# Kernel tuning notes

Measured on AMD Instinct MI355X. Metric: run time of the kernel, lower is better.

## Reference

```python
import jax, jax.numpy as jnp
import numpy as np

D_MODEL = 1024
HEAD = 16
EPS = 1e-6


def _norm(x, alpha, beta):
    # Faithful to NormalizeLayer: torch.std is unbiased (ddof=1); scalar alpha/bias.
    mean = jnp.mean(x, axis=-1, keepdims=True)
    std = jnp.std(x, axis=-1, ddof=1, keepdims=True)
    return alpha * ((x - mean) / (std + EPS)) + beta


def setup_inputs() -> dict:
    key = jax.random.key(0)
    ks = jax.random.split(key, 16)
    B, S, D = 4, 1024, D_MODEL
    s = 1.0 / np.sqrt(D)
    inp = {
        'x': jax.random.normal(ks[0], (B, S, D), dtype=jnp.float32),
        'mask': jnp.ones((B, 1, 1, S), dtype=jnp.int32),
        'Wq_w': jax.random.normal(ks[1], (D, D), dtype=jnp.float32) * s,
        'Wq_b': jnp.zeros((D,), dtype=jnp.float32),
        'Wk_w': jax.random.normal(ks[2], (D, D), dtype=jnp.float32) * s,
        'Wk_b': jnp.zeros((D,), dtype=jnp.float32),
        'Wv_w': jax.random.normal(ks[3], (D, D), dtype=jnp.float32) * s,
        'Wv_b': jnp.zeros((D,), dtype=jnp.float32),
        'Wo_w': jax.random.normal(ks[4], (D, D), dtype=jnp.float32) * s,
        'Wo_b': jnp.zeros((D,), dtype=jnp.float32),
        'ff1_w': jax.random.normal(ks[5], (D, D), dtype=jnp.float32) * s,
        'ff1_b': jnp.zeros((D,), dtype=jnp.float32),
        'ff2_w': jax.random.normal(ks[6], (D, D), dtype=jnp.float32) * s,
        'ff2_b': jnp.zeros((D,), dtype=jnp.float32),
        'alpha1': jnp.ones((1,), dtype=jnp.float32),
        'beta1': jnp.zeros((1,), dtype=jnp.float32),
        'alpha2': jnp.ones((1,), dtype=jnp.float32),
        'beta2': jnp.zeros((1,), dtype=jnp.float32),
    }
    return inp


def reference(x, mask, Wq_w, Wq_b, Wk_w, Wk_b, Wv_w, Wv_b, Wo_w, Wo_b,
              ff1_w, ff1_b, ff2_w, ff2_b, alpha1, beta1, alpha2, beta2):
    B, S, D = x.shape
    H = HEAD
    kd = D // H
    # QKV projections (torch Linear: y = x @ W.T + b)
    Q = (x @ Wq_w.T + Wq_b).reshape(B, S, H, kd).transpose(0, 2, 1, 3)
    K = (x @ Wk_w.T + Wk_b).reshape(B, S, H, kd).transpose(0, 2, 1, 3)
    V = (x @ Wv_w.T + Wv_b).reshape(B, S, H, kd).transpose(0, 2, 1, 3)
    score = jnp.einsum('bhqd,bhkd->bhqk', Q, K) / jnp.sqrt(jnp.float32(kd))
    score = jnp.where(mask == 0, -jnp.inf, score)
    attn = jax.nn.softmax(score, axis=-1)
    o = jnp.einsum('bhqk,bhkd->bhqd', attn, V)
    o = o.transpose(0, 2, 1, 3).reshape(B, S, D)
    attn_out = o @ Wo_w.T + Wo_b
    # residual 1 + custom norm (dropout is identity in eval / drop=0)
    x1 = _norm(x + attn_out, alpha1, beta1)
    # feed-forward: Linear -> ReLU -> Linear (both d_model x d_model)
    ff = jax.nn.relu(x1 @ ff1_w.T + ff1_b) @ ff2_w.T + ff2_b
    # residual 2 + custom norm
    return _norm(x1 + ff, alpha2, beta2)
```

## Files before the change

kernel.cpp:

```cpp
#include <hip/hip_runtime.h>


typedef __bf16 bf16x8 __attribute__((ext_vector_type(8)));
typedef float f32x4 __attribute__((ext_vector_type(4)));
typedef unsigned short ushort4v __attribute__((ext_vector_type(4)));

static __device__ __forceinline__ unsigned short f2bf(float f) {
  return __builtin_bit_cast(unsigned short, (__bf16)f);
}
static __device__ __forceinline__ float bf2f(unsigned short u) {
  return __builtin_bit_cast(float, (unsigned int)u << 16);
}

static __device__ __forceinline__ void gload_lds16(const void* g, void* l) {
  __builtin_amdgcn_global_load_lds(
      (const __attribute__((address_space(1))) unsigned int*)g,
      (__attribute__((address_space(3))) unsigned int*)l, 16, 0, 0);
}

__global__ __launch_bounds__(256)
void cvt_all(const float* __restrict__ x, const float* __restrict__ wq,
             const float* __restrict__ wk, const float* __restrict__ wv,
             const float* __restrict__ wo, const float* __restrict__ w1,
             const float* __restrict__ w2,
             unsigned short* __restrict__ x_bf, unsigned short* __restrict__ wqkv_bf,
             unsigned short* __restrict__ wo_bf, unsigned short* __restrict__ w1_bf,
             unsigned short* __restrict__ w2_bf) {
  const int y = blockIdx.y;
  const size_t MEL = 1u << 20;
  const float* src;
  unsigned short* dst;
  switch (y) {
    case 0: case 1: case 2: case 3: src = x + y * MEL; dst = x_bf + y * MEL; break;
    case 4: src = wq; dst = wqkv_bf; break;
    case 5: src = wk; dst = wqkv_bf + MEL; break;
    case 6: src = wv; dst = wqkv_bf + 2 * MEL; break;
    case 7: src = wo; dst = wo_bf; break;
    case 8: src = w1; dst = w1_bf; break;
    default: src = w2; dst = w2_bf; break;
  }
  const int i = blockIdx.x * 256 + threadIdx.x;
  const float4 v = reinterpret_cast<const float4*>(src)[i];
  ushort4v o;
  o[0] = f2bf(v.x); o[1] = f2bf(v.y); o[2] = f2bf(v.z); o[3] = f2bf(v.w);
  reinterpret_cast<ushort4v*>(dst)[i] = o;
}

template<bool RELU, int OUT_MODE>
__global__ __launch_bounds__(256, 2)
void gemm_bt(const unsigned short* __restrict__ A,
             const unsigned short* __restrict__ W,
             const float* __restrict__ bias0, const float* __restrict__ bias1,
             const float* __restrict__ bias2,
             void* __restrict__ out0, unsigned short* __restrict__ outK,
             unsigned short* __restrict__ outVt, int M, int N, int K) {
  __shared__ __align__(16) unsigned short Al[2][64][64];
  __shared__ __align__(16) unsigned short Bl[2][128][64];
  const int tid = threadIdx.x;
  const int lane = tid & 63;
  const int w = tid >> 6;
  const int wr = w >> 1, wc = w & 1;
  const int grp = lane >> 4, l15 = lane & 15;
  const long bRow = (long)blockIdx.x * 64;
  const long bCol = (long)blockIdx.y * 128;

  f32x4 acc[2][4];
#pragma unroll
  for (int m = 0; m < 2; m++)
#pragma unroll
    for (int n = 0; n < 4; n++) { f32x4 z = {0.f,0.f,0.f,0.f}; acc[m][n] = z; }

  const int srow = tid >> 3;
  const int xc = (((tid & 7) ^ (srow & 7)) << 3);
  const unsigned short* Ag0 = A + (bRow + srow) * (long)K + xc;
  const unsigned short* Ag1 = Ag0 + 32L * K;
  const unsigned short* Wg0 = W + (bCol + srow) * (long)K + xc;
  const unsigned short* Wg1 = Wg0 + 32L * K;
  const unsigned short* Wg2 = Wg0 + 64L * K;
  const unsigned short* Wg3 = Wg0 + 96L * K;

  auto stage = [&](int k0, int buf) {
    unsigned short* ldsA = &Al[buf][0][0] + w * 512;
    unsigned short* ldsB = &Bl[buf][0][0] + w * 512;
    gload_lds16(Ag0 + k0, ldsA);
    gload_lds16(Ag1 + k0, ldsA + 2048);
    gload_lds16(Wg0 + k0, ldsB);
    gload_lds16(Wg1 + k0, ldsB + 2048);
    gload_lds16(Wg2 + k0, ldsB + 4096);
    gload_lds16(Wg3 + k0, ldsB + 6144);
  };

  const int NT = K >> 6;
  stage(0, 0);
  for (int t = 0; t < NT; ++t) {
    const int cur = t & 1;
    __syncthreads();
    if (t + 1 < NT) stage((t + 1) << 6, cur ^ 1);
#pragma unroll
    for (int kk = 0; kk < 2; kk++) {
      bf16x8 af[2], bfr[4];
#pragma unroll
      for (int m = 0; m < 2; m++) {
        const int R = wr * 32 + m * 16 + l15;
        const int pos = (kk * 4 + grp) ^ (R & 7);
        af[m] = *(const bf16x8*)&Al[cur][R][pos << 3];
      }
#pragma unroll
      for (int n = 0; n < 4; n++) {
        const int R = wc * 64 + n * 16 + l15;
        const int pos = (kk * 4 + grp) ^ (R & 7);
        bfr[n] = *(const bf16x8*)&Bl[cur][R][pos << 3];
      }
#pragma unroll
      for (int m = 0; m < 2; m++)
#pragma unroll
        for (int n = 0; n < 4; n++)
          acc[m][n] = __builtin_amdgcn_mfma_f32_16x16x32_bf16(af[m], bfr[n], acc[m][n], 0, 0, 0);
    }
  }

  const float QSCL = 0.125f * 1.44269504088896340736f;
  const int seg = (OUT_MODE == 2) ? (int)(bCol >> 10) : 0;
  const float* bp = (OUT_MODE == 2) ? (seg == 0 ? bias0 : seg == 1 ? bias1 : bias2) : bias0;
#pragma unroll
  for (int n = 0; n < 4; n++) {
    const long col = bCol + wc * 64 + n * 16 + l15;
    const float bv = bp[OUT_MODE == 2 ? (col & 1023) : col];
#pragma unroll
    for (int m = 0; m < 2; m++) {
      const long row0 = bRow + wr * 32 + m * 16 + grp * 4;
#pragma unroll
      for (int r = 0; r < 4; r++) {
        float v = acc[m][n][r] + bv;
        if (RELU) v = fmaxf(v, 0.f);
        const long row = row0 + r;
        if (OUT_MODE == 1) {
          ((unsigned short*)out0)[row * (long)N + col] = f2bf(v);
        } else {
          if (seg == 0) {
            ((unsigned short*)out0)[row * 1024 + col] = f2bf(v * QSCL);
          } else if (seg == 1) {
            outK[row * 1024 + (col & 1023)] = f2bf(v);
          } else {
            const long vc = col & 1023;
            const long idx = (((row >> 10) * 16 + (vc >> 6)) << 16) + ((vc & 63) << 10) + (row & 1023);
            outVt[idx] = f2bf(v);
          }
        }
      }
    }
  }
}

__global__ __launch_bounds__(256, 2)
void attn_kernel(const unsigned short* __restrict__ Qb,
                 const unsigned short* __restrict__ Kb,
                 const unsigned short* __restrict__ Vt_g,
                 const int* __restrict__ maskp,
                 unsigned short* __restrict__ Ob) {
  const int S = 1024, D = 1024;
  __shared__ __align__(16) unsigned short Kl[2][64][64];
  __shared__ __align__(16) unsigned short Vl[2][64][64];
  __shared__ __align__(16) unsigned short Pl[128][64];
  const int tid = threadIdx.x;
  const int lane = tid & 63;
  const int w = tid >> 6;
  const int grp = lane >> 4, l15 = lane & 15;
  const int bh = blockIdx.x;
  const int qt = blockIdx.y;
  const int b = bh >> 4, h = bh & 15;
  const float NEG = -__builtin_inff();

  const int4 mv = *(const int4*)(maskp + b * S + tid * 4);
  const int allLive = __syncthreads_and(mv.x && mv.y && mv.z && mv.w);

  bf16x8 aq[2][2];
#pragma unroll
  for (int m = 0; m < 2; m++) {
    const unsigned short* Qp =
        Qb + ((size_t)(b * S + qt * 128 + w * 32 + m * 16 + l15)) * D + h * 64;
    aq[m][0] = *(const bf16x8*)(Qp + grp * 8);
    aq[m][1] = *(const bf16x8*)(Qp + 32 + grp * 8);
  }

  bf16x8 onesb;
#pragma unroll
  for (int j = 0; j < 8; j++) onesb[j] = (__bf16)1.0f;

  f32x4 acc_o[2][4];
#pragma unroll
  for (int m = 0; m < 2; m++)
#pragma unroll
    for (int f = 0; f < 4; f++) { f32x4 z = {0.f,0.f,0.f,0.f}; acc_o[m][f] = z; }
  f32x4 acc_l[2] = {{0.f,0.f,0.f,0.f}, {0.f,0.f,0.f,0.f}};
  float M = NEG;

  const int srow = tid >> 3;
  const int xc = (((tid & 7) ^ (srow & 7)) << 3);
  const unsigned short* Kg0 = Kb + ((size_t)(b * S + srow)) * D + h * 64 + xc;
  const unsigned short* Kg1 = Kg0 + 32 * (size_t)D;
  const unsigned short* Vgb = Vt_g + (((size_t)bh) << 16);
  const unsigned short* Vg0 = Vgb + (size_t)srow * S + xc;
  const unsigned short* Vg1 = Vg0 + 32 * (size_t)S;

  auto stage = [&](int kt2, int buf) {
    const size_t kb = (size_t)kt2 * 64;
    gload_lds16(Kg0 + kb * D, &Kl[buf][0][0] + w * 512);
    gload_lds16(Kg1 + kb * D, &Kl[buf][0][0] + w * 512 + 2048);
    gload_lds16(Vg0 + kb,     &Vl[buf][0][0] + w * 512);
    gload_lds16(Vg1 + kb,     &Vl[buf][0][0] + w * 512 + 2048);
  };
  stage(0, 0);

  for (int kt = 0; kt < 16; ++kt) {
    const int cur = kt & 1;
    const int kbase = kt * 64;
    __syncthreads();
    if (kt < 15) stage(kt + 1, cur ^ 1);

    f32x4 sfr[2][4];
    __builtin_amdgcn_s_setprio(1);
#pragma unroll
    for (int f = 0; f < 4; f++) {
      const int R = f * 16 + l15;
      const int p0 = (grp ^ (R & 7)) << 3;
      const int p1 = ((4 + grp) ^ (R & 7)) << 3;
      bf16x8 bk0 = *(const bf16x8*)&Kl[cur][R][p0];
      bf16x8 bk1 = *(const bf16x8*)&Kl[cur][R][p1];
#pragma unroll
      for (int m = 0; m < 2; m++) {
        f32x4 z = {0.f,0.f,0.f,0.f};
        z = __builtin_amdgcn_mfma_f32_16x16x32_bf16(aq[m][0], bk0, z, 0, 0, 0);
        z = __builtin_amdgcn_mfma_f32_16x16x32_bf16(aq[m][1], bk1, z, 0, 0, 0);
        sfr[m][f] = z;
      }
    }
    __builtin_amdgcn_s_setprio(0);

    if (!allLive) {
#pragma unroll
      for (int f = 0; f < 4; f++) {
        const float biasf = maskp[b * S + kbase + f * 16 + l15] ? 0.f : NEG;
#pragma unroll
        for (int m = 0; m < 2; m++)
#pragma unroll
          for (int r = 0; r < 4; r++) sfr[m][f][r] += biasf;
      }
    }

    float rm = sfr[0][0][0];
#pragma unroll
    for (int m = 0; m < 2; m++)
#pragma unroll
      for (int f = 0; f < 4; f++)
#pragma unroll
        for (int r = 0; r < 4; r++) rm = fmaxf(rm, sfr[m][f][r]);
    rm = fmaxf(rm, __shfl_xor(rm, 1));
    rm = fmaxf(rm, __shfl_xor(rm, 2));
    rm = fmaxf(rm, __shfl_xor(rm, 4));
    rm = fmaxf(rm, __shfl_xor(rm, 8));
    rm = fmaxf(rm, __shfl_xor(rm, 16));
    rm = fmaxf(rm, __shfl_xor(rm, 32));
    if (rm > M + 8.f) {
      const float sc = exp2f(M - rm);
      M = rm;
#pragma unroll
      for (int m = 0; m < 2; m++) {
#pragma unroll
        for (int f = 0; f < 4; f++) acc_o[m][f] *= sc;
        acc_l[m] *= sc;
      }
    }

#pragma unroll
    for (int m = 0; m < 2; m++)
#pragma unroll
      for (int f = 0; f < 4; f++)
#pragma unroll
        for (int r = 0; r < 4; r++) {
          const float p = exp2f(sfr[m][f][r] - M);
          const int q = w * 32 + m * 16 + grp * 4 + r;
          const int cchunk = (f * 2 + (l15 >> 3)) ^ (q & 7);
          ((unsigned short*)Pl)[q * 64 + (cchunk << 3) + (l15 & 7)] = f2bf(p);
        }

    bf16x8 bv0[4], bv1[4];
#pragma unroll
    for (int f = 0; f < 4; f++) {
      const int Rv = f * 16 + l15;
      bv0[f] = *(const bf16x8*)&Vl[cur][Rv][((grp ^ (Rv & 7)) << 3)];
      bv1[f] = *(const bf16x8*)&Vl[cur][Rv][(((4 + grp) ^ (Rv & 7)) << 3)];
    }

    __builtin_amdgcn_s_setprio(1);
#pragma unroll
    for (int m = 0; m < 2; m++) {
      const int Rp = w * 32 + m * 16 + l15;
      const bf16x8 ap0 = *(const bf16x8*)&Pl[Rp][((grp ^ (Rp & 7)) << 3)];
      const bf16x8 ap1 = *(const bf16x8*)&Pl[Rp][(((4 + grp) ^ (Rp & 7)) << 3)];
#pragma unroll
      for (int f = 0; f < 4; f++) {
        acc_o[m][f] = __builtin_amdgcn_mfma_f32_16x16x32_bf16(ap0, bv0[f], acc_o[m][f], 0, 0, 0);
        acc_o[m][f] = __builtin_amdgcn_mfma_f32_16x16x32_bf16(ap1, bv1[f], acc_o[m][f], 0, 0, 0);
      }
      acc_l[m] = __builtin_amdgcn_mfma_f32_16x16x32_bf16(ap0, onesb, acc_l[m], 0, 0, 0);
      acc_l[m] = __builtin_amdgcn_mfma_f32_16x16x32_bf16(ap1, onesb, acc_l[m], 0, 0, 0);
    }
    __builtin_amdgcn_s_setprio(0);
  }

#pragma unroll
  for (int m = 0; m < 2; m++)
#pragma unroll
    for (int r = 0; r < 4; r++) {
      const float inv = 1.f / acc_l[m][r];
      const int row = qt * 128 + w * 32 + m * 16 + grp * 4 + r;
#pragma unroll
      for (int f = 0; f < 4; f++) {
        const float v = acc_o[m][f][r] * inv;
        Ob[((size_t)(b * S + row)) * D + h * 64 + f * 16 + l15] = f2bf(v);
      }
    }
}

template<int AMODE, int BMODE, bool F32OUT, bool BF16OUT>
__global__ __launch_bounds__(256)
void norm_residual(const void* __restrict__ a, const void* __restrict__ bsrc,
                   const float* __restrict__ alpha, const float* __restrict__ beta,
                   float* __restrict__ out, unsigned short* __restrict__ out_bf) {
  const int D = 1024;
  const size_t base = (size_t)blockIdx.x * D + threadIdx.x * 4;
  float a0, a1, a2, a3, b0v, b1v, b2v, b3v;
  if (AMODE == 0) {
    const float4 va = *(const float4*)((const float*)a + base);
    a0 = va.x; a1 = va.y; a2 = va.z; a3 = va.w;
  } else {
    const ushort4v va = *(const ushort4v*)((const unsigned short*)a + base);
    a0 = bf2f(va[0]); a1 = bf2f(va[1]); a2 = bf2f(va[2]); a3 = bf2f(va[3]);
  }
  if (BMODE == 0) {
    const float4 vb = *(const float4*)((const float*)bsrc + base);
    b0v = vb.x; b1v = vb.y; b2v = vb.z; b3v = vb.w;
  } else {
    const ushort4v vb = *(const ushort4v*)((const unsigned short*)bsrc + base);
    b0v = bf2f(vb[0]); b1v = bf2f(vb[1]); b2v = bf2f(vb[2]); b3v = bf2f(vb[3]);
  }
  const float x0 = a0 + b0v, x1 = a1 + b1v, x2 = a2 + b2v, x3 = a3 + b3v;
  float s1 = x0 + x1 + x2 + x3;
  float s2 = x0 * x0 + x1 * x1 + x2 * x2 + x3 * x3;
#pragma unroll
  for (int m = 1; m < 64; m <<= 1) {
    s1 += __shfl_xor(s1, m);
    s2 += __shfl_xor(s2, m);
  }
  __shared__ float red[8];
  const int w = threadIdx.x >> 6, lane = threadIdx.x & 63;
  if (lane == 0) { red[w] = s1; red[4 + w] = s2; }
  __syncthreads();
  s1 = red[0] + red[1] + red[2] + red[3];
  s2 = red[4] + red[5] + red[6] + red[7];
  const float mean = s1 * (1.f / 1024.f);
  const float var = fmaxf((s2 - 1024.f * mean * mean) * (1.f / 1023.f), 0.f);
  const float k = alpha[0] / (sqrtf(var) + 1e-6f);
  const float b0 = beta[0];
  const float y0 = (x0 - mean) * k + b0;
  const float y1 = (x1 - mean) * k + b0;
  const float y2 = (x2 - mean) * k + b0;
  const float y3 = (x3 - mean) * k + b0;
  if (F32OUT) {
    float4 o = {y0, y1, y2, y3};
    *(float4*)(out + base) = o;
  }
  if (BF16OUT) {
    ushort4v ob;
    ob[0] = f2bf(y0); ob[1] = f2bf(y1); ob[2] = f2bf(y2); ob[3] = f2bf(y3);
    *(ushort4v*)(out_bf + base) = ob;
  }
}

extern "C" void kernel_launch(void* const* d_in, const int* in_sizes, int n_in,
                              void* d_out, int out_size, void* d_ws, size_t ws_size,
                              hipStream_t stream) {
  const float* x      = (const float*)d_in[0];
  const int*   maskp  = (const int*)d_in[1];
  const float* Wq_w   = (const float*)d_in[2];
  const float* Wq_b   = (const float*)d_in[3];
  const float* Wk_w   = (const float*)d_in[4];
  const float* Wk_b   = (const float*)d_in[5];
  const float* Wv_w   = (const float*)d_in[6];
  const float* Wv_b   = (const float*)d_in[7];
  const float* Wo_w   = (const float*)d_in[8];
  const float* Wo_b   = (const float*)d_in[9];
  const float* W1_w   = (const float*)d_in[10];
  const float* W1_b   = (const float*)d_in[11];
  const float* W2_w   = (const float*)d_in[12];
  const float* W2_b   = (const float*)d_in[13];
  const float* alpha1 = (const float*)d_in[14];
  const float* beta1  = (const float*)d_in[15];
  const float* alpha2 = (const float*)d_in[16];
  const float* beta2  = (const float*)d_in[17];

  const int B = 4, S = 1024, D = 1024;
  const int M = B * S;
  const size_t MiB = 1u << 20;
  char* ws = (char*)d_ws;
  unsigned short* x_bf    = (unsigned short*)(ws + 0 * MiB);
  unsigned short* Wqkv_bf = (unsigned short*)(ws + 8 * MiB);
  unsigned short* Wo_bf   = (unsigned short*)(ws + 14 * MiB);
  unsigned short* W1_bf   = (unsigned short*)(ws + 16 * MiB);
  unsigned short* W2_bf   = (unsigned short*)(ws + 18 * MiB);
  unsigned short* Q_bf    = (unsigned short*)(ws + 20 * MiB);
  unsigned short* K_bf    = (unsigned short*)(ws + 28 * MiB);
  unsigned short* Vt_bf   = (unsigned short*)(ws + 36 * MiB);
  unsigned short* O_bf    = (unsigned short*)(ws + 44 * MiB);
  unsigned short* attn_bf = (unsigned short*)(ws + 52 * MiB);
  unsigned short* x1_bf   = (unsigned short*)(ws + 20 * MiB);
  unsigned short* ff1_bf  = (unsigned short*)(ws + 28 * MiB);
  unsigned short* ff2_bf  = (unsigned short*)(ws + 36 * MiB);

  cvt_all<<<dim3(1024, 10), dim3(256), 0, stream>>>(
      x, Wq_w, Wk_w, Wv_w, Wo_w, W1_w, W2_w, x_bf, Wqkv_bf, Wo_bf, W1_bf, W2_bf);

  gemm_bt<false, 2><<<dim3(M / 64, 24), dim3(256), 0, stream>>>(
      x_bf, Wqkv_bf, Wq_b, Wk_b, Wv_b, Q_bf, K_bf, Vt_bf, M, 3072, D);

  attn_kernel<<<dim3(B * 16, S / 128), dim3(256), 0, stream>>>(Q_bf, K_bf, Vt_bf, maskp, O_bf);

  gemm_bt<false, 1><<<dim3(M / 64, 8), dim3(256), 0, stream>>>(
      O_bf, Wo_bf, Wo_b, nullptr, nullptr, attn_bf, nullptr, nullptr, M, D, D);
  norm_residual<0, 1, false, true><<<dim3(M), dim3(256), 0, stream>>>(
      x, attn_bf, alpha1, beta1, nullptr, x1_bf);
  gemm_bt<true, 1><<<dim3(M / 64, 8), dim3(256), 0, stream>>>(
      x1_bf, W1_bf, W1_b, nullptr, nullptr, ff1_bf, nullptr, nullptr, M, D, D);
  gemm_bt<false, 1><<<dim3(M / 64, 8), dim3(256), 0, stream>>>(
      ff1_bf, W2_bf, W2_b, nullptr, nullptr, ff2_bf, nullptr, nullptr, M, D, D);
  norm_residual<1, 1, true, false><<<dim3(M), dim3(256), 0, stream>>>(
      x1_bf, ff2_bf, alpha2, beta2, (float*)d_out, nullptr);
}
```

Baseline: 158.3 us.

## Stage GEMM and attention outputs through LDS for coalesced stores, fuse residual adds

The GEMM epilogue now writes its tile into shared memory and then stores it with 16-byte vectorized rows, including a transposed staging path for the V^T layout. The attention kernel also stages its output through LDS before storing it the same way. The residual add moves into the Wo and FF2 GEMM epilogues, so the norm kernels read a single bf16 input. This is meant to replace scattered 2-byte global stores and cut one input read per norm, at the cost of extra LDS traffic, syncs and per-element residual loads in the epilogue. The first residual (x in fp32) is now rounded to bf16 before the norm, which is a small precision change.

After: 167.1 us. 5.5% more time.

```diff
diff --git a/kernel.cpp b/kernel.cpp
--- a/kernel.cpp
+++ b/kernel.cpp
@@ -4,6 +4,7 @@
 typedef __bf16 bf16x8 __attribute__((ext_vector_type(8)));
 typedef float f32x4 __attribute__((ext_vector_type(4)));
 typedef unsigned short ushort4v __attribute__((ext_vector_type(4)));
+typedef unsigned short ushort8v __attribute__((ext_vector_type(8)));
 
 static __device__ __forceinline__ unsigned short f2bf(float f) {
   return __builtin_bit_cast(unsigned short, (__bf16)f);
@@ -52,6 +53,7 @@
              const unsigned short* __restrict__ W,
              const float* __restrict__ bias0, const float* __restrict__ bias1,
              const float* __restrict__ bias2,
+             const void* __restrict__ res,
              void* __restrict__ out0, unsigned short* __restrict__ outK,
              unsigned short* __restrict__ outVt, int M, int N, int K) {
   __shared__ __align__(16) unsigned short Al[2][64][64];
@@ -122,33 +124,56 @@
   const float QSCL = 0.125f * 1.44269504088896340736f;
   const int seg = (OUT_MODE == 2) ? (int)(bCol >> 10) : 0;
   const float* bp = (OUT_MODE == 2) ? (seg == 0 ? bias0 : seg == 1 ? bias1 : bias2) : bias0;
+  unsigned short* Cl = &Al[0][0][0];
+  __syncthreads();
 #pragma unroll
   for (int n = 0; n < 4; n++) {
-    const long col = bCol + wc * 64 + n * 16 + l15;
+    const int cc = wc * 64 + n * 16 + l15;
+    const long col = bCol + cc;
     const float bv = bp[OUT_MODE == 2 ? (col & 1023) : col];
 #pragma unroll
     for (int m = 0; m < 2; m++) {
-      const long row0 = bRow + wr * 32 + m * 16 + grp * 4;
+      const int row0 = wr * 32 + m * 16 + grp * 4;
 #pragma unroll
       for (int r = 0; r < 4; r++) {
+        const int rl = row0 + r;
         float v = acc[m][n][r] + bv;
         if (RELU) v = fmaxf(v, 0.f);
-        const long row = row0 + r;
-        if (OUT_MODE == 1) {
-          ((unsigned short*)out0)[row * (long)N + col] = f2bf(v);
-        } else {
-          if (seg == 0) {
-            ((unsigned short*)out0)[row * 1024 + col] = f2bf(v * QSCL);
-          } else if (seg == 1) {
-            outK[row * 1024 + (col & 1023)] = f2bf(v);
-          } else {
-            const long vc = col & 1023;
-            const long idx = (((row >> 10) * 16 + (vc >> 6)) << 16) + ((vc & 63) << 10) + (row & 1023);
-            outVt[idx] = f2bf(v);
-          }
-        }
-      }
-    }
+        if (OUT_MODE == 3)
+          v += ((const float*)res)[(bRow + rl) * (long)N + col];
+        if (OUT_MODE == 4)
+          v += bf2f(((const unsigned short*)res)[(bRow + rl) * (long)N + col]);
+        if (OUT_MODE == 2 && seg == 0) v *= QSCL;
+        if (OUT_MODE == 2 && seg == 2) Cl[cc * 64 + rl] = f2bf(v);
+        else                           Cl[rl * 128 + cc] = f2bf(v);
+      }
+    }
+  }
+  __syncthreads();
+  if (OUT_MODE == 2 && seg == 2) {
+    const int cc = tid >> 1;
+    const int sh = tid & 1;
+    const long bidx = (bRow >> 10) * 16 + ((((long)(bCol & 1023)) + cc) >> 6);
+    unsigned short* dst = outVt + (bidx << 16) + ((long)(cc & 63) << 10) +
+                          (bRow & 1023) + sh * 32;
+    const unsigned short* srcp = Cl + cc * 64 + sh * 32;
+#pragma unroll
+    for (int k = 0; k < 4; k++)
+      *(ushort8v*)(dst + k * 8) = *(const ushort8v*)(srcp + k * 8);
+  } else {
+    const int rl = tid >> 2;
+    const int q = tid & 3;
+    const unsigned short* srcp = Cl + rl * 128 + q * 32;
+    unsigned short* dst;
+    if (OUT_MODE == 2) {
+      if (seg == 0) dst = (unsigned short*)out0 + (bRow + rl) * 1024 + bCol + q * 32;
+      else          dst = outK + (bRow + rl) * 1024 + (bCol - 1024) + q * 32;
+    } else {
+      dst = (unsigned short*)out0 + (bRow + rl) * (long)N + bCol + q * 32;
+    }
+#pragma unroll
+    for (int k = 0; k < 4; k++)
+      *(ushort8v*)(dst + k * 8) = *(const ushort8v*)(srcp + k * 8);
   }
 }
 
@@ -309,43 +334,39 @@
     __builtin_amdgcn_s_setprio(0);
   }
 
+  __syncthreads();
+  unsigned short* Ol = &Pl[0][0];
 #pragma unroll
   for (int m = 0; m < 2; m++)
 #pragma unroll
     for (int r = 0; r < 4; r++) {
       const float inv = 1.f / acc_l[m][r];
-      const int row = qt * 128 + w * 32 + m * 16 + grp * 4 + r;
-#pragma unroll
-      for (int f = 0; f < 4; f++) {
-        const float v = acc_o[m][f][r] * inv;
-        Ob[((size_t)(b * S + row)) * D + h * 64 + f * 16 + l15] = f2bf(v);
-      }
-    }
-}
-
-template<int AMODE, int BMODE, bool F32OUT, bool BF16OUT>
+      const int row = w * 32 + m * 16 + grp * 4 + r;
+#pragma unroll
+      for (int f = 0; f < 4; f++)
+        Ol[row * 64 + f * 16 + l15] = f2bf(acc_o[m][f][r] * inv);
+    }
+  __syncthreads();
+  {
+    const int row = tid >> 1;
+    const int half = tid & 1;
+    const unsigned short* srcp = Ol + row * 64 + half * 32;
+    unsigned short* dst = Ob + ((size_t)(b * S + qt * 128 + row)) * D + h * 64 + half * 32;
+#pragma unroll
+    for (int k = 0; k < 4; k++)
+      *(ushort8v*)(dst + k * 8) = *(const ushort8v*)(srcp + k * 8);
+  }
+}
+
+template<bool F32OUT>
 __global__ __launch_bounds__(256)
-void norm_residual(const void* __restrict__ a, const void* __restrict__ bsrc,
-                   const float* __restrict__ alpha, const float* __restrict__ beta,
-                   float* __restrict__ out, unsigned short* __restrict__ out_bf) {
+void norm_single(const unsigned short* __restrict__ s,
+                 const float* __restrict__ alpha, const float* __restrict__ beta,
+                 float* __restrict__ out, unsigned short* __restrict__ out_bf) {
   const int D = 1024;
   const size_t base = (size_t)blockIdx.x * D + threadIdx.x * 4;
-  float a0, a1, a2, a3, b0v, b1v, b2v, b3v;
-  if (AMODE == 0) {
-    const float4 va = *(const float4*)((const float*)a + base);
-    a0 = va.x; a1 = va.y; a2 = va.z; a3 = va.w;
-  } else {
-    const ushort4v va = *(const ushort4v*)((const unsigned short*)a + base);
-    a0 = bf2f(va[0]); a1 = bf2f(va[1]); a2 = bf2f(va[2]); a3 = bf2f(va[3]);
-  }
-  if (BMODE == 0) {
-    const float4 vb = *(const float4*)((const float*)bsrc + base);
-    b0v = vb.x; b1v = vb.y; b2v = vb.z; b3v = vb.w;
-  } else {
-    const ushort4v vb = *(const ushort4v*)((const unsigned short*)bsrc + base);
-    b0v = bf2f(vb[0]); b1v = bf2f(vb[1]); b2v = bf2f(vb[2]); b3v = bf2f(vb[3]);
-  }
-  const float x0 = a0 + b0v, x1 = a1 + b1v, x2 = a2 + b2v, x3 = a3 + b3v;
+  const ushort4v vs = *(const ushort4v*)(s + base);
+  const float x0 = bf2f(vs[0]), x1 = bf2f(vs[1]), x2 = bf2f(vs[2]), x3 = bf2f(vs[3]);
   float s1 = x0 + x1 + x2 + x3;
   float s2 = x0 * x0 + x1 * x1 + x2 * x2 + x3 * x3;
 #pragma unroll
@@ -370,8 +391,7 @@
   if (F32OUT) {
     float4 o = {y0, y1, y2, y3};
     *(float4*)(out + base) = o;
-  }
-  if (BF16OUT) {
+  } else {
     ushort4v ob;
     ob[0] = f2bf(y0); ob[1] = f2bf(y1); ob[2] = f2bf(y2); ob[3] = f2bf(y3);
     *(ushort4v*)(out_bf + base) = ob;
@@ -413,27 +433,26 @@
   unsigned short* K_bf    = (unsigned short*)(ws + 28 * MiB);
   unsigned short* Vt_bf   = (unsigned short*)(ws + 36 * MiB);
   unsigned short* O_bf    = (unsigned short*)(ws + 44 * MiB);
-  unsigned short* attn_bf = (unsigned short*)(ws + 52 * MiB);
+  unsigned short* s1_bf   = (unsigned short*)(ws + 52 * MiB);
   unsigned short* x1_bf   = (unsigned short*)(ws + 20 * MiB);
   unsigned short* ff1_bf  = (unsigned short*)(ws + 28 * MiB);
-  unsigned short* ff2_bf  = (unsigned short*)(ws + 36 * MiB);
+  unsigned short* s2_bf   = (unsigned short*)(ws + 36 * MiB);
 
   cvt_all<<<dim3(1024, 10), dim3(256), 0, stream>>>(
       x, Wq_w, Wk_w, Wv_w, Wo_w, W1_w, W2_w, x_bf, Wqkv_bf, Wo_bf, W1_bf, W2_bf);
 
   gemm_bt<false, 2><<<dim3(M / 64, 24), dim3(256), 0, stream>>>(
-      x_bf, Wqkv_bf, Wq_b, Wk_b, Wv_b, Q_bf, K_bf, Vt_bf, M, 3072, D);
+      x_bf, Wqkv_bf, Wq_b, Wk_b, Wv_b, nullptr, Q_bf, K_bf, Vt_bf, M, 3072, D);
 
   attn_kernel<<<dim3(B * 16, S / 128), dim3(256), 0, stream>>>(Q_bf, K_bf, Vt_bf, maskp, O_bf);
 
-  gemm_bt<false, 1><<<dim3(M / 64, 8), dim3(256), 0, stream>>>(
-      O_bf, Wo_bf, Wo_b, nullptr, nullptr, attn_bf, nullptr, nullptr, M, D, D);
-  norm_residual<0, 1, false, true><<<dim3(M), dim3(256), 0, stream>>>(
-      x, attn_bf, alpha1, beta1, nullptr, x1_bf);
+  gemm_bt<false, 3><<<dim3(M / 64, 8), dim3(256), 0, stream>>>(
+      O_bf, Wo_bf, Wo_b, nullptr, nullptr, x, s1_bf, nullptr, nullptr, M, D, D);
+  norm_single<false><<<dim3(M), dim3(256), 0, stream>>>(s1_bf, alpha1, beta1, nullptr, x1_bf);
   gemm_bt<true, 1><<<dim3(M / 64, 8), dim3(256), 0, stream>>>(
-      x1_bf, W1_bf, W1_b, nullptr, nullptr, ff1_bf, nullptr, nullptr, M, D, D);
-  gemm_bt<false, 1><<<dim3(M / 64, 8), dim3(256), 0, stream>>>(
-      ff1_bf, W2_bf, W2_b, nullptr, nullptr, ff2_bf, nullptr, nullptr, M, D, D);
-  norm_residual<1, 1, true, false><<<dim3(M), dim3(256), 0, stream>>>(
-      x1_bf, ff2_bf, alpha2, beta2, (float*)d_out, nullptr);
-}
+      x1_bf, W1_bf, W1_b, nullptr, nullptr, nullptr, ff1_bf, nullptr, nullptr, M, D, D);
+  gemm_bt<false, 4><<<dim3(M / 64, 8), dim3(256), 0, stream>>>(
+      ff1_bf, W2_bf, W2_b, nullptr, nullptr, x1_bf, s2_bf, nullptr, nullptr, M, D, D);
+  norm_single<true><<<dim3(M), dim3(256), 0, stream>>>(s2_bf, alpha2, beta2,
+                                                       (float*)d_out, nullptr);
+}
```
